# Performance work log

Hardware: AMD Instinct MI355X
Metric: run time of the kernel (lower is better)

The kernel has to match this reference:

```python
import jax, jax.numpy as jnp
import numpy as np

SIGMA_D = 1.0  # init kwarg sigma_d
# d_model = 2 -> div_term = exp(arange(0,2,2) * (-ln(10000)/2)) = [1.0]


def setup_inputs() -> dict:
    key = jax.random.key(0)
    k0, k1 = jax.random.split(key)
    B, N, M = 4, 3000, 3000
    points0 = jax.random.normal(k0, (B, N, 2), dtype=jnp.float32)
    points1 = jax.random.normal(k1, (B, M, 2), dtype=jnp.float32)
    return {"points0": points0, "points1": points1}


def reference(points0, points1):
    # pairwise distance with points_normlize=True: sq_dist = clamp(2 - 2*<p0,p1>, 0)
    xy = jnp.einsum('bnc,bmc->bnm', points0, points1)  # (B,N,M)
    sq_dist = jnp.clip(2.0 - 2.0 * xy, 0.0)
    d_indices = jnp.sqrt(sq_dist) / SIGMA_D  # (B,N,M)
    # sinusoidal embedding with d_model=2, div_term=[1.0] -> [sin(d), cos(d)]
    d_embeddings = jnp.stack([jnp.sin(d_indices), jnp.cos(d_indices)], axis=-1)  # (B,N,M,2)
    d_embeddings = jax.lax.stop_gradient(d_embeddings)  # torch detaches + no_grad
    # einsum 'bnc,bnmc->bnc': multiply by sum over m
    points0_emb = points0 * d_embeddings.sum(axis=2)  # (B,N,2)
    # einsum 'bmc,bmnc->bmc' with permuted emb: sum over n
    points1_emb = points1 * d_embeddings.sum(axis=1)  # (B,M,2)
    return (points0_emb, points1_emb)
```

## Files before the change

kernel.cpp:

```cpp
#include <hip/hip_runtime.h>
#include <math.h>


#define GB 4
#define GN 3000
#define NT 47
#define TPB (NT * NT)
#define INV2PI 0.15915494309189535f

#define WS_FLOATS (2 * GB * GN * 2)

__device__ __forceinline__ float bperm(int addr, float x) {
    return __int_as_float(__builtin_amdgcn_ds_bpermute(addr, __float_as_int(x)));
}

__global__ __launch_bounds__(256) void geo_tile_kernel(
    const float* __restrict__ p0,
    const float* __restrict__ p1,
    float* __restrict__ ws)
{
    const int lane = threadIdx.x & 63;
    const int wid  = (blockIdx.x << 2) | (threadIdx.x >> 6);

    int b   = wid / TPB;
    int rem = wid - b * TPB;
    int rt  = rem / NT;
    int ct  = rem - rt * NT;

    const int rbase = rt << 6;
    const int cbase = ct << 6;

    int rl = rbase + lane; if (rl >= GN) rl = GN - 1;
    int cl = cbase + lane; if (cl >= GN) cl = GN - 1;

    const float2 pr = ((const float2*)p0)[b * GN + rl];
    const float2 qq = ((const float2*)p1)[b * GN + cl];
    const float px = pr.x, py = pr.y;
    float qx = qq.x, qy = qq.y;

    const int perm = ((lane + 1) & 63) << 2;

    float rs = 0.f, rc = 0.f;
    float cs = 0.f, cc = 0.f;

    const bool full = (rbase + 64 <= GN) && (cbase + 64 <= GN);

    if (full) {
        #pragma unroll 8
        for (int j = 0; j < 64; ++j) {
            float dot = fmaf(px, qx, py * qy);
            float t   = fmaxf(fmaf(-2.0f, dot, 2.0f), 0.0f);
            float d   = __builtin_amdgcn_sqrtf(t);
            float r   = d * INV2PI;
            float s   = __builtin_amdgcn_sinf(r);
            float c   = __builtin_amdgcn_cosf(r);
            rs += s;  rc += c;
            cs += s;  cc += c;
            qx = bperm(perm, qx);
            qy = bperm(perm, qy);
            cs = bperm(perm, cs);
            cc = bperm(perm, cc);
        }
    } else {
        const float rowv = (rbase + lane < GN) ? 1.0f : 0.0f;
        float colv = (cbase + lane < GN) ? 1.0f : 0.0f;
        #pragma unroll 4
        for (int j = 0; j < 64; ++j) {
            float dot = fmaf(px, qx, py * qy);
            float t   = fmaxf(fmaf(-2.0f, dot, 2.0f), 0.0f);
            float d   = __builtin_amdgcn_sqrtf(t);
            float r   = d * INV2PI;
            float s   = __builtin_amdgcn_sinf(r) * rowv;
            float c   = __builtin_amdgcn_cosf(r) * rowv;
            rs = fmaf(s, colv, rs);
            rc = fmaf(c, colv, rc);
            cs += s;  cc += c;
            qx = bperm(perm, qx);
            qy = bperm(perm, qy);
            cs = bperm(perm, cs);
            cc = bperm(perm, cc);
            colv = bperm(perm, colv);
        }
    }

    if (rbase + lane < GN) {
        float* wr = ws + (b * GN + rbase + lane) * 2;
        unsafeAtomicAdd(wr + 0, rs);
        unsafeAtomicAdd(wr + 1, rc);
    }
    if (cbase + lane < GN) {
        float* wc = ws + (GB * GN + b * GN + cbase + lane) * 2;
        unsafeAtomicAdd(wc + 0, cs);
        unsafeAtomicAdd(wc + 1, cc);
    }
}

__global__ __launch_bounds__(256) void geo_epilogue_kernel(
    const float* __restrict__ p0,
    const float* __restrict__ p1,
    const float* __restrict__ ws,
    float* __restrict__ out)
{
    const int i = blockIdx.x * 256 + threadIdx.x;
    const int ROWS = GB * GN;
    if (i >= 2 * ROWS) return;
    const float2 pr = (i < ROWS) ? ((const float2*)p0)[i]
                                 : ((const float2*)p1)[i - ROWS];
    const float2 w = ((const float2*)ws)[i];
    float2 res;
    res.x = pr.x * w.x;
    res.y = pr.y * w.y;
    ((float2*)out)[i] = res;
}

extern "C" void kernel_launch(void* const* d_in, const int* in_sizes, int n_in,
                              void* d_out, int out_size, void* d_ws, size_t ws_size,
                              hipStream_t stream) {
    const float* points0 = (const float*)d_in[0];
    const float* points1 = (const float*)d_in[1];
    float* out = (float*)d_out;
    float* ws = (float*)d_ws;

    hipMemsetAsync(ws, 0, WS_FLOATS * sizeof(float), stream);

    const int nblocks = (GB * TPB) / 4 + ((GB * TPB) % 4 ? 1 : 0);
    geo_tile_kernel<<<dim3(nblocks), dim3(256), 0, stream>>>(points0, points1, ws);

    const int rows2 = 2 * GB * GN;
    geo_epilogue_kernel<<<dim3((rows2 + 255) / 256), dim3(256), 0, stream>>>(
        points0, points1, ws, out);
}
```

Measured before the change: 85.19 us.

## Use DPP row rotation and per-tile partials instead of bpermute and atomics

The tile kernel now rotates column data within 16-lane rows using DPP moves instead of LDS bpermute. It processes 64 columns as four groups of 16 and combines column sums across rows with xor shuffles. Global atomics and the workspace memset are replaced by per-tile partial sums written to a padded workspace. A reduce kernel then sums the 47 partials per point. This trades atomic traffic and LDS permutes for extra workspace memory and reduction reads.

Measured after the change: 84.20 us. Within noise of the previous version (-1.2%).

```diff
diff --git a/kernel.cpp b/kernel.cpp
--- a/kernel.cpp
+++ b/kernel.cpp
@@ -5,16 +5,18 @@
 #define GB 4
 #define GN 3000
 #define NT 47
+#define PAD 3008
 #define TPB (NT * NT)
 #define INV2PI 0.15915494309189535f
 
-#define WS_FLOATS (2 * GB * GN * 2)
+#define WSROW_F2 (GB * NT * PAD)
 
-__device__ __forceinline__ float bperm(int addr, float x) {
-    return __int_as_float(__builtin_amdgcn_ds_bpermute(addr, __float_as_int(x)));
+__device__ __forceinline__ float rot1(float x) {
+    return __int_as_float(__builtin_amdgcn_mov_dpp(
+        __float_as_int(x), 0x121 , 0xF, 0xF, true));
 }
 
-__global__ __launch_bounds__(256) void geo_tile_kernel(
+__global__ __launch_bounds__(256) void geo_dpp_kernel(
     const float* __restrict__ p0,
     const float* __restrict__ p1,
     float* __restrict__ ws)
@@ -27,75 +29,80 @@
     int rt  = rem / NT;
     int ct  = rem - rt * NT;
 
-    const int rbase = rt << 6;
-    const int cbase = ct << 6;
+    const int r = (rt << 6) + lane;
+    const int rload = (r < GN) ? r : (GN - 1);
+    const float2 pr = ((const float2*)p0)[b * GN + rload];
+    const float px2 = -2.0f * pr.x;
+    const float py2 = -2.0f * pr.y;
 
-    int rl = rbase + lane; if (rl >= GN) rl = GN - 1;
-    int cl = cbase + lane; if (cl >= GN) cl = GN - 1;
+    float rs = 0.0f, rc = 0.0f;
 
-    const float2 pr = ((const float2*)p0)[b * GN + rl];
-    const float2 qq = ((const float2*)p1)[b * GN + cl];
-    const float px = pr.x, py = pr.y;
-    float qx = qq.x, qy = qq.y;
+    float2* __restrict__ wrow = (float2*)ws + (b * NT + ct) * PAD;
+    float2* __restrict__ wcol = (float2*)ws + WSROW_F2 + (b * NT + rt) * PAD;
 
-    const int perm = ((lane + 1) & 63) << 2;
-
-    float rs = 0.f, rc = 0.f;
-    float cs = 0.f, cc = 0.f;
-
-    const bool full = (rbase + 64 <= GN) && (cbase + 64 <= GN);
+    const bool full = (rt < NT - 1) && (ct < NT - 1);
 
     if (full) {
-        #pragma unroll 8
-        for (int j = 0; j < 64; ++j) {
-            float dot = fmaf(px, qx, py * qy);
-            float t   = fmaxf(fmaf(-2.0f, dot, 2.0f), 0.0f);
-            float d   = __builtin_amdgcn_sqrtf(t);
-            float r   = d * INV2PI;
-            float s   = __builtin_amdgcn_sinf(r);
-            float c   = __builtin_amdgcn_cosf(r);
-            rs += s;  rc += c;
-            cs += s;  cc += c;
-            qx = bperm(perm, qx);
-            qy = bperm(perm, qy);
-            cs = bperm(perm, cs);
-            cc = bperm(perm, cc);
+        #pragma unroll
+        for (int g = 0; g < 4; ++g) {
+            const int cidx = (ct << 6) + (g << 4) + (lane & 15);
+            const float2 qq = ((const float2*)p1)[b * GN + cidx];
+            float qx = qq.x, qy = qq.y;
+            float cs = 0.0f, cc = 0.0f;
+            #pragma unroll
+            for (int j = 0; j < 16; ++j) {
+                float t = fmaf(px2, qx, fmaf(py2, qy, 2.0f));
+                t = fmaxf(t, 0.0f);
+                float d = __builtin_amdgcn_sqrtf(t);
+                float rr = d * INV2PI;
+                float s = __builtin_amdgcn_sinf(rr);
+                float c = __builtin_amdgcn_cosf(rr);
+                rs += s;  rc += c;
+                cs += s;  cc += c;
+                qx = rot1(qx);  qy = rot1(qy);
+                cs = rot1(cs);  cc = rot1(cc);
+            }
+            cs += __shfl_xor(cs, 16, 64);  cs += __shfl_xor(cs, 32, 64);
+            cc += __shfl_xor(cc, 16, 64);  cc += __shfl_xor(cc, 32, 64);
+            if (lane < 16)
+                wcol[(ct << 6) + (g << 4) + lane] = make_float2(cs, cc);
         }
     } else {
-        const float rowv = (rbase + lane < GN) ? 1.0f : 0.0f;
-        float colv = (cbase + lane < GN) ? 1.0f : 0.0f;
-        #pragma unroll 4
-        for (int j = 0; j < 64; ++j) {
-            float dot = fmaf(px, qx, py * qy);
-            float t   = fmaxf(fmaf(-2.0f, dot, 2.0f), 0.0f);
-            float d   = __builtin_amdgcn_sqrtf(t);
-            float r   = d * INV2PI;
-            float s   = __builtin_amdgcn_sinf(r) * rowv;
-            float c   = __builtin_amdgcn_cosf(r) * rowv;
-            rs = fmaf(s, colv, rs);
-            rc = fmaf(c, colv, rc);
-            cs += s;  cc += c;
-            qx = bperm(perm, qx);
-            qy = bperm(perm, qy);
-            cs = bperm(perm, cs);
-            cc = bperm(perm, cc);
-            colv = bperm(perm, colv);
+        const float rowv = (r < GN) ? 1.0f : 0.0f;
+        #pragma unroll
+        for (int g = 0; g < 4; ++g) {
+            const int cidx0 = (ct << 6) + (g << 4) + (lane & 15);
+            const int cidx  = (cidx0 < GN) ? cidx0 : (GN - 1);
+            const float2 qq = ((const float2*)p1)[b * GN + cidx];
+            float qx = qq.x, qy = qq.y;
+            float colv = (cidx0 < GN) ? 1.0f : 0.0f;
+            float cs = 0.0f, cc = 0.0f;
+            #pragma unroll
+            for (int j = 0; j < 16; ++j) {
+                float t = fmaf(px2, qx, fmaf(py2, qy, 2.0f));
+                t = fmaxf(t, 0.0f);
+                float d = __builtin_amdgcn_sqrtf(t);
+                float rr = d * INV2PI;
+                float s = __builtin_amdgcn_sinf(rr) * rowv;
+                float c = __builtin_amdgcn_cosf(rr) * rowv;
+                rs = fmaf(s, colv, rs);
+                rc = fmaf(c, colv, rc);
+                cs += s;  cc += c;
+                qx = rot1(qx);  qy = rot1(qy);
+                cs = rot1(cs);  cc = rot1(cc);
+                colv = rot1(colv);
+            }
+            cs += __shfl_xor(cs, 16, 64);  cs += __shfl_xor(cs, 32, 64);
+            cc += __shfl_xor(cc, 16, 64);  cc += __shfl_xor(cc, 32, 64);
+            if (lane < 16)
+                wcol[(ct << 6) + (g << 4) + lane] = make_float2(cs, cc);
         }
     }
 
-    if (rbase + lane < GN) {
-        float* wr = ws + (b * GN + rbase + lane) * 2;
-        unsafeAtomicAdd(wr + 0, rs);
-        unsafeAtomicAdd(wr + 1, rc);
-    }
-    if (cbase + lane < GN) {
-        float* wc = ws + (GB * GN + b * GN + cbase + lane) * 2;
-        unsafeAtomicAdd(wc + 0, cs);
-        unsafeAtomicAdd(wc + 1, cc);
-    }
+    wrow[r < PAD ? r : PAD - 1] = make_float2(rs, rc);
 }
 
-__global__ __launch_bounds__(256) void geo_epilogue_kernel(
+__global__ __launch_bounds__(256) void geo_reduce_kernel(
     const float* __restrict__ p0,
     const float* __restrict__ p1,
     const float* __restrict__ ws,
@@ -104,12 +111,29 @@
     const int i = blockIdx.x * 256 + threadIdx.x;
     const int ROWS = GB * GN;
     if (i >= 2 * ROWS) return;
-    const float2 pr = (i < ROWS) ? ((const float2*)p0)[i]
-                                 : ((const float2*)p1)[i - ROWS];
-    const float2 w = ((const float2*)ws)[i];
+
+    const bool side0 = (i < ROWS);
+    const int idx = side0 ? i : i - ROWS;
+    const int b = idx / GN;
+    const int r = idx - b * GN;
+
+    const float2* base = side0
+        ? (const float2*)ws + (b * NT) * PAD + r
+        : (const float2*)ws + WSROW_F2 + (b * NT) * PAD + r;
+
+    float sx = 0.0f, sy = 0.0f;
+    #pragma unroll 8
+    for (int t = 0; t < NT; ++t) {
+        float2 v = base[t * PAD];
+        sx += v.x;
+        sy += v.y;
+    }
+
+    const float2 p = side0 ? ((const float2*)p0)[idx]
+                           : ((const float2*)p1)[idx];
     float2 res;
-    res.x = pr.x * w.x;
-    res.y = pr.y * w.y;
+    res.x = p.x * sx;
+    res.y = p.y * sy;
     ((float2*)out)[i] = res;
 }
 
@@ -121,12 +145,10 @@
     float* out = (float*)d_out;
     float* ws = (float*)d_ws;
 
-    hipMemsetAsync(ws, 0, WS_FLOATS * sizeof(float), stream);
-
-    const int nblocks = (GB * TPB) / 4 + ((GB * TPB) % 4 ? 1 : 0);
-    geo_tile_kernel<<<dim3(nblocks), dim3(256), 0, stream>>>(points0, points1, ws);
+    const int nblocks = (GB * TPB + 3) / 4;
+    geo_dpp_kernel<<<dim3(nblocks), dim3(256), 0, stream>>>(points0, points1, ws);
 
     const int rows2 = 2 * GB * GN;
-    geo_epilogue_kernel<<<dim3((rows2 + 255) / 256), dim3(256), 0, stream>>>(
+    geo_reduce_kernel<<<dim3((rows2 + 255) / 256), dim3(256), 0, stream>>>(
         points0, points1, ws, out);
 }
```
